# Optimization experiments

Hardware: AMD Instinct MI355X
Metric: run time of the kernel (lower is better)

The kernel has to match this reference:

```python
import jax, jax.numpy as jnp
import numpy as np

N, E, H, C = 50000, 800000, 4, 32   # nodes, edges, heads, per-head channels
HID, LAT, G = H * C, 32, 128        # hidden, latent, num graphs
IN_DIM = 64
NEG_SLOPE = 0.2
BN_EPS = 1e-5


def setup_inputs() -> dict:
    key = jax.random.key(0)
    ks = jax.random.split(key, 20)
    inp = {
        "x": jax.random.normal(ks[0], (N, IN_DIM), jnp.float32),
        "edge_index": jax.random.randint(ks[1], (2, E), 0, N, jnp.int32),
        "batch": jnp.sort(jax.random.randint(ks[2], (N,), 0, G, jnp.int32)),
        # layer 0
        "W0": jax.random.normal(ks[3], (IN_DIM, HID), jnp.float32) * (1.0 / np.sqrt(IN_DIM)),
        "a_src0": jax.random.normal(ks[4], (H, C), jnp.float32) * 0.1,
        "a_dst0": jax.random.normal(ks[5], (H, C), jnp.float32) * 0.1,
        "b0": jnp.zeros((HID,), jnp.float32),
        # layer 1
        "W1": jax.random.normal(ks[6], (HID, HID), jnp.float32) * (1.0 / np.sqrt(HID)),
        "a_src1": jax.random.normal(ks[7], (H, C), jnp.float32) * 0.1,
        "a_dst1": jax.random.normal(ks[8], (H, C), jnp.float32) * 0.1,
        "b1": jnp.zeros((HID,), jnp.float32),
        # layer 2
        "W2": jax.random.normal(ks[9], (HID, HID), jnp.float32) * (1.0 / np.sqrt(HID)),
        "a_src2": jax.random.normal(ks[10], (H, C), jnp.float32) * 0.1,
        "a_dst2": jax.random.normal(ks[11], (H, C), jnp.float32) * 0.1,
        "b2": jnp.zeros((HID,), jnp.float32),
        # head
        "fc_w": jax.random.normal(ks[12], (HID, LAT), jnp.float32) * (1.0 / np.sqrt(HID)),
        "fc_b": jnp.zeros((LAT,), jnp.float32),
        "bn_g": jnp.ones((LAT,), jnp.float32),
        "bn_b": jnp.zeros((LAT,), jnp.float32),
    }
    return inp


def _gat_conv(x, src, dst, W, a_src, a_dst, b):
    n = x.shape[0]
    h = (x @ W).reshape(n, H, C)                      # [N,H,C]
    alpha_s = jnp.einsum("nhc,hc->nh", h, a_src)       # [N,H]
    alpha_d = jnp.einsum("nhc,hc->nh", h, a_dst)
    e = jax.nn.leaky_relu(alpha_s[src] + alpha_d[dst], NEG_SLOPE)  # [E',H]
    # scatter-softmax over incoming edges of each dst node
    m = jax.ops.segment_max(e, dst, num_segments=n)
    m = jnp.where(jnp.isfinite(m), m, 0.0)
    ex = jnp.exp(e - m[dst])
    denom = jax.ops.segment_sum(ex, dst, num_segments=n)
    alpha = ex / (denom[dst] + 1e-16)                  # [E',H]
    out = jax.ops.segment_sum(alpha[:, :, None] * h[src], dst, num_segments=n)
    return out.reshape(n, H * C) + b


def reference(x, edge_index, batch, W0, a_src0, a_dst0, b0, W1, a_src1, a_dst1, b1,
              W2, a_src2, a_dst2, b2, fc_w, fc_b, bn_g, bn_b):
    # PyG GATConv default add_self_loops=True
    loop = jnp.arange(N, dtype=edge_index.dtype)
    src = jnp.concatenate([edge_index[0], loop])
    dst = jnp.concatenate([edge_index[1], loop])

    h = x
    for (W, a_s, a_d, b) in ((W0, a_src0, a_dst0, b0),
                             (W1, a_src1, a_dst1, b1),
                             (W2, a_src2, a_dst2, b2)):
        h = _gat_conv(h, src, dst, W, a_s, a_d, b)
        h = jax.nn.leaky_relu(h, NEG_SLOPE)  # dropout is identity in eval

    pooled = jax.ops.segment_sum(h, batch, num_segments=G)  # global_add_pool -> [G,HID]
    out = pooled @ fc_w + fc_b
    # BatchNorm1d in eval mode with running_mean=0, running_var=1
    out = bn_g * out * (1.0 / np.sqrt(1.0 + BN_EPS)) + bn_b
    return out
```

## Files before the change

kernel.cpp:

```cpp
#include <hip/hip_runtime.h>
#include <hip/hip_bf16.h>
#include <float.h>

#define NEG 0.2f

__device__ __forceinline__ float leaky(float x) { return x > 0.0f ? x : NEG * x; }

__device__ __forceinline__ unsigned short f2bf(float f) {
  unsigned x = __float_as_uint(f);
  unsigned r = (x + 0x7fffu + ((x >> 16) & 1u)) >> 16;
  return (unsigned short)r;
}

__device__ __forceinline__ float2 bf2f2(unsigned u) {
  float2 r;
  r.x = __uint_as_float(u << 16);
  r.y = __uint_as_float(u & 0xffff0000u);
  return r;
}

__global__ void zero_kernel(int* __restrict__ p, int n) {
  int i = blockIdx.x * blockDim.x + threadIdx.x;
  int stride = gridDim.x * blockDim.x;
  for (; i < n; i += stride) p[i] = 0;
}

__global__ void count_kernel(const int* __restrict__ ei, int* __restrict__ deg, int E, int N) {
  int i = blockIdx.x * blockDim.x + threadIdx.x;
  if (i >= E + N) return;
  int dst = (i < E) ? ei[E + i] : (i - E);
  atomicAdd(&deg[dst], 1);
}

__global__ __launch_bounds__(1024) void scan_block_kernel(const int* __restrict__ deg,
                                                          int* __restrict__ row_start,
                                                          int* __restrict__ sums, int n) {
  __shared__ int buf[1024];
  int t = threadIdx.x;
  int idx = blockIdx.x * 1024 + t;
  int x = (idx < n) ? deg[idx] : 0;
  int v = x;
  buf[t] = v;
  __syncthreads();
  for (int off = 1; off < 1024; off <<= 1) {
    int a = (t >= off) ? buf[t - off] : 0;
    __syncthreads();
    v += a;
    buf[t] = v;
    __syncthreads();
  }
  if (idx < n) row_start[idx] = v - x;
  if (t == 1023) sums[blockIdx.x] = v;
}

__global__ __launch_bounds__(1024) void scan_sums_kernel(int* __restrict__ sums,
                                                         int* __restrict__ row_start,
                                                         int nch, int n) {
  __shared__ int buf[1024];
  int t = threadIdx.x;
  int x = (t < nch) ? sums[t] : 0;
  int v = x;
  buf[t] = v;
  __syncthreads();
  for (int off = 1; off < 1024; off <<= 1) {
    int a = (t >= off) ? buf[t - off] : 0;
    __syncthreads();
    v += a;
    buf[t] = v;
    __syncthreads();
  }
  if (t < nch) sums[t] = v - x;
  if (t == 1023) row_start[n] = v;
}

__global__ __launch_bounds__(1024) void scan_add_kernel(int* __restrict__ row_start,
                                                        const int* __restrict__ sums, int n) {
  int idx = blockIdx.x * 1024 + threadIdx.x;
  if (idx < n) row_start[idx] += sums[blockIdx.x];
}

__global__ void fill_kernel(const int* __restrict__ ei, int* __restrict__ cursor,
                            const int* __restrict__ row_start, int* __restrict__ csr_src,
                            int* __restrict__ csr_dst, int E, int N) {
  int i = blockIdx.x * blockDim.x + threadIdx.x;
  if (i >= E + N) return;
  int src, dst;
  if (i < E) { src = ei[i]; dst = ei[E + i]; } else { src = dst = i - E; }
  int pos = atomicAdd(&cursor[dst], 1);
  int slot = row_start[dst] + pos;
  csr_src[slot] = src;
  csr_dst[slot] = dst;
}

__global__ __launch_bounds__(256) void gemm_kernel(const float* __restrict__ X,
                                                   const float* __restrict__ W,
                                                   unsigned short* __restrict__ Hb,
                                                   const float* __restrict__ a_src,
                                                   const float* __restrict__ a_dst,
                                                   float* __restrict__ as_arr,
                                                   float* __restrict__ ad_arr,
                                                   int nrows, int K) {
  __shared__ float Xs[64][36];
  __shared__ float Ws[32][132];
  int t = threadIdx.x;
  int row0 = blockIdx.x * 64;
  int tcol = t & 31;
  int trow = t >> 5;
  float acc[8][4];
#pragma unroll
  for (int i = 0; i < 8; ++i)
#pragma unroll
    for (int j = 0; j < 4; ++j) acc[i][j] = 0.0f;

  for (int kb = 0; kb < K; kb += 32) {
#pragma unroll
    for (int p = 0; p < 2; ++p) {
      int flat = t + p * 256;
      int r = flat >> 3;
      int kq = (flat & 7) * 4;
      float4 v = make_float4(0.f, 0.f, 0.f, 0.f);
      int gr = row0 + r;
      if (gr < nrows) v = *(const float4*)(X + (size_t)gr * K + kb + kq);
      *(float4*)(&Xs[r][kq]) = v;
    }
#pragma unroll
    for (int p = 0; p < 4; ++p) {
      int flat = t + p * 256;
      int r = flat >> 5;
      int cq = (flat & 31) * 4;
      float4 v = *(const float4*)(W + (size_t)(kb + r) * 128 + cq);
      *(float4*)(&Ws[r][cq]) = v;
    }
    __syncthreads();
#pragma unroll
    for (int kk = 0; kk < 32; kk += 4) {
      float4 xv[8];
#pragma unroll
      for (int i = 0; i < 8; ++i) xv[i] = *(const float4*)(&Xs[trow + 8 * i][kk]);
#pragma unroll
      for (int q = 0; q < 4; ++q) {
        float4 wv = *(const float4*)(&Ws[kk + q][tcol * 4]);
#pragma unroll
        for (int i = 0; i < 8; ++i) {
          float xq = (q == 0) ? xv[i].x : (q == 1) ? xv[i].y : (q == 2) ? xv[i].z : xv[i].w;
          acc[i][0] += xq * wv.x;
          acc[i][1] += xq * wv.y;
          acc[i][2] += xq * wv.z;
          acc[i][3] += xq * wv.w;
        }
      }
    }
    __syncthreads();
  }

  float4 as4 = *(const float4*)(a_src + tcol * 4);
  float4 ad4 = *(const float4*)(a_dst + tcol * 4);
  float ps[8], pd[8];
#pragma unroll
  for (int i = 0; i < 8; ++i) {
    int r = row0 + trow + 8 * i;
    if (r < nrows) {
      union { unsigned short u[4]; uint2 v; } pk;
      pk.u[0] = f2bf(acc[i][0]);
      pk.u[1] = f2bf(acc[i][1]);
      pk.u[2] = f2bf(acc[i][2]);
      pk.u[3] = f2bf(acc[i][3]);
      *(uint2*)(Hb + (size_t)r * 128 + tcol * 4) = pk.v;
    }
    ps[i] = acc[i][0] * as4.x + acc[i][1] * as4.y + acc[i][2] * as4.z + acc[i][3] * as4.w;
    pd[i] = acc[i][0] * ad4.x + acc[i][1] * ad4.y + acc[i][2] * ad4.z + acc[i][3] * ad4.w;
  }
#pragma unroll
  for (int off = 1; off < 8; off <<= 1) {
#pragma unroll
    for (int i = 0; i < 8; ++i) {
      ps[i] += __shfl_xor(ps[i], off);
      pd[i] += __shfl_xor(pd[i], off);
    }
  }
  if ((tcol & 7) == 0) {
    int head = tcol >> 3;
#pragma unroll
    for (int i = 0; i < 8; ++i) {
      int r = row0 + trow + 8 * i;
      if (r < nrows) {
        as_arr[(size_t)r * 4 + head] = ps[i];
        ad_arr[(size_t)r * 4 + head] = pd[i];
      }
    }
  }
}

__global__ __launch_bounds__(256) void ecomp_kernel(const int* __restrict__ csr_src,
                                                    const int* __restrict__ csr_dst,
                                                    const float* __restrict__ as_arr,
                                                    const float* __restrict__ ad_arr,
                                                    float* __restrict__ earr, int Etot) {
  int i = blockIdx.x * 256 + threadIdx.x;
  if (i >= Etot) return;
  int s = csr_src[i];
  int d = csr_dst[i];
  float4 a = *(const float4*)(as_arr + (size_t)s * 4);
  float4 b = *(const float4*)(ad_arr + (size_t)d * 4);
  float4 e;
  e.x = __expf(fminf(leaky(a.x + b.x), 80.f));
  e.y = __expf(fminf(leaky(a.y + b.y), 80.f));
  e.z = __expf(fminf(leaky(a.z + b.z), 80.f));
  e.w = __expf(fminf(leaky(a.w + b.w), 80.f));
  *(float4*)(earr + (size_t)i * 4) = e;
}

template <int POOL>
__global__ __launch_bounds__(256) void agg_kernel(const unsigned short* __restrict__ Hb,
                                                  const float* __restrict__ earr,
                                                  const int* __restrict__ csr_src,
                                                  const int* __restrict__ row_start,
                                                  const float* __restrict__ bias,
                                                  float* __restrict__ xnext,
                                                  const int* __restrict__ batch,
                                                  float* __restrict__ pooled, int N) {
  int wid = threadIdx.x >> 6;
  int lane = threadIdx.x & 63;
  int n = blockIdx.x * 4 + wid;
  if (n >= N) return;
  int rs = row_start[n], re = row_start[n + 1];
  int head = lane >> 4;

  const unsigned* hp = (const unsigned*)Hb + lane;
  const float* ep = earr + head;
  float denom = 0.f, acc0 = 0.f, acc1 = 0.f;
  int i = rs;
  for (; i + 4 <= re; i += 4) {
    int s0 = csr_src[i], s1 = csr_src[i + 1], s2 = csr_src[i + 2], s3 = csr_src[i + 3];
    float e0 = ep[(size_t)i * 4];
    float e1 = ep[(size_t)(i + 1) * 4];
    float e2 = ep[(size_t)(i + 2) * 4];
    float e3 = ep[(size_t)(i + 3) * 4];
    unsigned u0 = hp[(size_t)s0 * 64];
    unsigned u1 = hp[(size_t)s1 * 64];
    unsigned u2 = hp[(size_t)s2 * 64];
    unsigned u3 = hp[(size_t)s3 * 64];
    denom += (e0 + e1) + (e2 + e3);
    float2 f;
    f = bf2f2(u0); acc0 += e0 * f.x; acc1 += e0 * f.y;
    f = bf2f2(u1); acc0 += e1 * f.x; acc1 += e1 * f.y;
    f = bf2f2(u2); acc0 += e2 * f.x; acc1 += e2 * f.y;
    f = bf2f2(u3); acc0 += e3 * f.x; acc1 += e3 * f.y;
  }
  for (; i < re; ++i) {
    int s0 = csr_src[i];
    float e0 = ep[(size_t)i * 4];
    unsigned u0 = hp[(size_t)s0 * 64];
    float2 f = bf2f2(u0);
    denom += e0;
    acc0 += e0 * f.x;
    acc1 += e0 * f.y;
  }
  float inv = 1.0f / (denom + 1e-16f);
  float2 bv = *(const float2*)(bias + 2 * lane);
  float v0 = leaky(acc0 * inv + bv.x);
  float v1 = leaky(acc1 * inv + bv.y);
  if (POOL) {
    int g = batch[n];
    atomicAdd(&pooled[(size_t)g * 128 + 2 * lane], v0);
    atomicAdd(&pooled[(size_t)g * 128 + 2 * lane + 1], v1);
  } else {
    *(float2*)(xnext + (size_t)n * 128 + 2 * lane) = make_float2(v0, v1);
  }
}

__global__ void head_kernel(const float* __restrict__ pooled, const float* __restrict__ fc_w,
                            const float* __restrict__ fc_b, const float* __restrict__ bn_g,
                            const float* __restrict__ bn_b, float* __restrict__ out, int G) {
  int t = threadIdx.x;
  int g = blockIdx.x * 8 + (t >> 5);
  int j = t & 31;
  if (g >= G) return;
  const float* pr = pooled + (size_t)g * 128;
  float acc = 0.f;
#pragma unroll 8
  for (int k = 0; k < 128; ++k) acc += pr[k] * fc_w[k * 32 + j];
  const float inv = 0.9999950000374997f;
  out[g * 32 + j] = bn_g[j] * (acc + fc_b[j]) * inv + bn_b[j];
}

extern "C" void kernel_launch(void* const* d_in, const int* in_sizes, int n_in,
                              void* d_out, int out_size, void* d_ws, size_t ws_size,
                              hipStream_t stream) {
  const float* x = (const float*)d_in[0];
  const int* ei = (const int*)d_in[1];
  const int* batch = (const int*)d_in[2];
  const float* Wm[3] = {(const float*)d_in[3], (const float*)d_in[7], (const float*)d_in[11]};
  const float* a_s[3] = {(const float*)d_in[4], (const float*)d_in[8], (const float*)d_in[12]};
  const float* a_d[3] = {(const float*)d_in[5], (const float*)d_in[9], (const float*)d_in[13]};
  const float* bb[3] = {(const float*)d_in[6], (const float*)d_in[10], (const float*)d_in[14]};
  const float* fc_w = (const float*)d_in[15];
  const float* fc_b = (const float*)d_in[16];
  const float* bn_g = (const float*)d_in[17];
  const float* bn_b = (const float*)d_in[18];
  float* out = (float*)d_out;

  int N = in_sizes[0] / 64;
  int E = in_sizes[1] / 2;
  int G = out_size / 32;
  int Etot = E + N;

  char* p = (char*)d_ws;
  auto carve = [&](size_t bytes) {
    char* r = p;
    p += (bytes + 255) & ~size_t(255);
    return r;
  };
  int* deg       = (int*)carve((size_t)N * 4);
  int* cursor    = (int*)carve((size_t)N * 4);
  float* pooled  = (float*)carve((size_t)G * 128 * 4);
  int* row_start = (int*)carve((size_t)(N + 1) * 4);
  int* sums      = (int*)carve(4096);
  int* csr_src   = (int*)carve((size_t)Etot * 4);
  int* csr_dst   = (int*)carve((size_t)Etot * 4);
  float* earr    = (float*)carve((size_t)Etot * 4 * 4);
  unsigned short* Hb = (unsigned short*)carve((size_t)N * 128 * 2);
  float* bufX    = (float*)carve((size_t)N * 128 * 4);
  float* as_arr  = (float*)carve((size_t)N * 4 * 4);
  float* ad_arr  = (float*)carve((size_t)N * 4 * 4);

  int nz = (int)(((char*)(pooled + (size_t)G * 128) - (char*)deg) / 4);
  zero_kernel<<<512, 256, 0, stream>>>(deg, nz);

  int egrid = (Etot + 255) / 256;
  count_kernel<<<egrid, 256, 0, stream>>>(ei, deg, E, N);
  int nch = (N + 1023) / 1024;
  scan_block_kernel<<<nch, 1024, 0, stream>>>(deg, row_start, sums, N);
  scan_sums_kernel<<<1, 1024, 0, stream>>>(sums, row_start, nch, N);
  scan_add_kernel<<<nch, 1024, 0, stream>>>(row_start, sums, N);
  fill_kernel<<<egrid, 256, 0, stream>>>(ei, cursor, row_start, csr_src, csr_dst, E, N);

  int ggrid = (N + 63) / 64;
  int ngrid = (N + 3) / 4;

  gemm_kernel<<<ggrid, 256, 0, stream>>>(x, Wm[0], Hb, a_s[0], a_d[0], as_arr, ad_arr, N, 64);
  ecomp_kernel<<<egrid, 256, 0, stream>>>(csr_src, csr_dst, as_arr, ad_arr, earr, Etot);
  agg_kernel<0><<<ngrid, 256, 0, stream>>>(Hb, earr, csr_src, row_start, bb[0],
                                           bufX, nullptr, nullptr, N);
  gemm_kernel<<<ggrid, 256, 0, stream>>>(bufX, Wm[1], Hb, a_s[1], a_d[1], as_arr, ad_arr, N, 128);
  ecomp_kernel<<<egrid, 256, 0, stream>>>(csr_src, csr_dst, as_arr, ad_arr, earr, Etot);
  agg_kernel<0><<<ngrid, 256, 0, stream>>>(Hb, earr, csr_src, row_start, bb[1],
                                           bufX, nullptr, nullptr, N);
  gemm_kernel<<<ggrid, 256, 0, stream>>>(bufX, Wm[2], Hb, a_s[2], a_d[2], as_arr, ad_arr, N, 128);
  ecomp_kernel<<<egrid, 256, 0, stream>>>(csr_src, csr_dst, as_arr, ad_arr, earr, Etot);
  agg_kernel<1><<<ngrid, 256, 0, stream>>>(Hb, earr, csr_src, row_start, bb[2],
                                           nullptr, batch, pooled, N);

  head_kernel<<<(G + 7) / 8, 256, 0, stream>>>(pooled, fc_w, fc_b, bn_g, bn_b, out, G);
}
```

Baseline: 483.1 us.

## Store features and edge weights head-major; aggregate per head with edge-parallel lanes

```diff
diff --git a/kernel.cpp b/kernel.cpp
--- a/kernel.cpp
+++ b/kernel.cpp
@@ -94,7 +94,7 @@
 
 __global__ __launch_bounds__(256) void gemm_kernel(const float* __restrict__ X,
                                                    const float* __restrict__ W,
-                                                   unsigned short* __restrict__ Hb,
+                                                   unsigned short* __restrict__ Hbh,
                                                    const float* __restrict__ a_src,
                                                    const float* __restrict__ a_dst,
                                                    float* __restrict__ as_arr,
@@ -155,6 +155,7 @@
 
   float4 as4 = *(const float4*)(a_src + tcol * 4);
   float4 ad4 = *(const float4*)(a_dst + tcol * 4);
+  int head = tcol >> 3, sub = tcol & 7;
   float ps[8], pd[8];
 #pragma unroll
   for (int i = 0; i < 8; ++i) {
@@ -165,7 +166,7 @@
       pk.u[1] = f2bf(acc[i][1]);
       pk.u[2] = f2bf(acc[i][2]);
       pk.u[3] = f2bf(acc[i][3]);
-      *(uint2*)(Hb + (size_t)r * 128 + tcol * 4) = pk.v;
+      *(uint2*)(Hbh + ((size_t)head * nrows + r) * 32 + sub * 4) = pk.v;
     }
     ps[i] = acc[i][0] * as4.x + acc[i][1] * as4.y + acc[i][2] * as4.z + acc[i][3] * as4.w;
     pd[i] = acc[i][0] * ad4.x + acc[i][1] * ad4.y + acc[i][2] * ad4.z + acc[i][3] * ad4.w;
@@ -178,8 +179,7 @@
       pd[i] += __shfl_xor(pd[i], off);
     }
   }
-  if ((tcol & 7) == 0) {
-    int head = tcol >> 3;
+  if (sub == 0) {
 #pragma unroll
     for (int i = 0; i < 8; ++i) {
       int r = row0 + trow + 8 * i;
@@ -195,77 +195,72 @@
                                                     const int* __restrict__ csr_dst,
                                                     const float* __restrict__ as_arr,
                                                     const float* __restrict__ ad_arr,
-                                                    float* __restrict__ earr, int Etot) {
+                                                    float* __restrict__ eh, int Etot) {
   int i = blockIdx.x * 256 + threadIdx.x;
   if (i >= Etot) return;
   int s = csr_src[i];
   int d = csr_dst[i];
   float4 a = *(const float4*)(as_arr + (size_t)s * 4);
   float4 b = *(const float4*)(ad_arr + (size_t)d * 4);
-  float4 e;
-  e.x = __expf(fminf(leaky(a.x + b.x), 80.f));
-  e.y = __expf(fminf(leaky(a.y + b.y), 80.f));
-  e.z = __expf(fminf(leaky(a.z + b.z), 80.f));
-  e.w = __expf(fminf(leaky(a.w + b.w), 80.f));
-  *(float4*)(earr + (size_t)i * 4) = e;
+  eh[i]                    = __expf(fminf(leaky(a.x + b.x), 80.f));
+  eh[(size_t)Etot + i]     = __expf(fminf(leaky(a.y + b.y), 80.f));
+  eh[(size_t)2 * Etot + i] = __expf(fminf(leaky(a.z + b.z), 80.f));
+  eh[(size_t)3 * Etot + i] = __expf(fminf(leaky(a.w + b.w), 80.f));
 }
 
 template <int POOL>
-__global__ __launch_bounds__(256) void agg_kernel(const unsigned short* __restrict__ Hb,
-                                                  const float* __restrict__ earr,
+__global__ __launch_bounds__(256) void agg_kernel(const unsigned short* __restrict__ Hbh,
+                                                  const float* __restrict__ eh,
                                                   const int* __restrict__ csr_src,
                                                   const int* __restrict__ row_start,
                                                   const float* __restrict__ bias,
                                                   float* __restrict__ xnext,
                                                   const int* __restrict__ batch,
-                                                  float* __restrict__ pooled, int N) {
+                                                  float* __restrict__ pooled,
+                                                  int N, int Etot) {
   int wid = threadIdx.x >> 6;
   int lane = threadIdx.x & 63;
+  int q = lane >> 4, ql = lane & 15;
   int n = blockIdx.x * 4 + wid;
   if (n >= N) return;
   int rs = row_start[n], re = row_start[n + 1];
-  int head = lane >> 4;
-
-  const unsigned* hp = (const unsigned*)Hb + lane;
-  const float* ep = earr + head;
-  float denom = 0.f, acc0 = 0.f, acc1 = 0.f;
-  int i = rs;
-  for (; i + 4 <= re; i += 4) {
-    int s0 = csr_src[i], s1 = csr_src[i + 1], s2 = csr_src[i + 2], s3 = csr_src[i + 3];
-    float e0 = ep[(size_t)i * 4];
-    float e1 = ep[(size_t)(i + 1) * 4];
-    float e2 = ep[(size_t)(i + 2) * 4];
-    float e3 = ep[(size_t)(i + 3) * 4];
-    unsigned u0 = hp[(size_t)s0 * 64];
-    unsigned u1 = hp[(size_t)s1 * 64];
-    unsigned u2 = hp[(size_t)s2 * 64];
-    unsigned u3 = hp[(size_t)s3 * 64];
-    denom += (e0 + e1) + (e2 + e3);
-    float2 f;
-    f = bf2f2(u0); acc0 += e0 * f.x; acc1 += e0 * f.y;
-    f = bf2f2(u1); acc0 += e1 * f.x; acc1 += e1 * f.y;
-    f = bf2f2(u2); acc0 += e2 * f.x; acc1 += e2 * f.y;
-    f = bf2f2(u3); acc0 += e3 * f.x; acc1 += e3 * f.y;
-  }
-  for (; i < re; ++i) {
-    int s0 = csr_src[i];
-    float e0 = ep[(size_t)i * 4];
-    unsigned u0 = hp[(size_t)s0 * 64];
-    float2 f = bf2f2(u0);
-    denom += e0;
-    acc0 += e0 * f.x;
-    acc1 += e0 * f.y;
-  }
-  float inv = 1.0f / (denom + 1e-16f);
-  float2 bv = *(const float2*)(bias + 2 * lane);
-  float v0 = leaky(acc0 * inv + bv.x);
-  float v1 = leaky(acc1 * inv + bv.y);
-  if (POOL) {
-    int g = batch[n];
-    atomicAdd(&pooled[(size_t)g * 128 + 2 * lane], v0);
-    atomicAdd(&pooled[(size_t)g * 128 + 2 * lane + 1], v1);
-  } else {
-    *(float2*)(xnext + (size_t)n * 128 + 2 * lane) = make_float2(v0, v1);
+  int g = POOL ? batch[n] : 0;
+
+#pragma unroll
+  for (int h = 0; h < 4; ++h) {
+    const unsigned* hb = (const unsigned*)Hbh + (size_t)h * N * 16 + ql;
+    const float* ep = eh + (size_t)h * Etot;
+    float acc0 = 0.f, acc1 = 0.f, den = 0.f;
+    for (int i = rs; i < re; i += 8) {
+      int i0 = i + q, i1 = i + 4 + q;
+      int j0 = i0 < re ? i0 : rs;
+      int j1 = i1 < re ? i1 : rs;
+      int s0 = csr_src[j0], s1 = csr_src[j1];
+      float e0 = i0 < re ? ep[j0] : 0.f;
+      float e1 = i1 < re ? ep[j1] : 0.f;
+      unsigned u0 = hb[(size_t)s0 * 16];
+      unsigned u1 = hb[(size_t)s1 * 16];
+      float2 f0 = bf2f2(u0), f1 = bf2f2(u1);
+      den += e0 + e1;
+      acc0 += e0 * f0.x + e1 * f1.x;
+      acc1 += e0 * f0.y + e1 * f1.y;
+    }
+    acc0 += __shfl_xor(acc0, 16); acc0 += __shfl_xor(acc0, 32);
+    acc1 += __shfl_xor(acc1, 16); acc1 += __shfl_xor(acc1, 32);
+    den  += __shfl_xor(den, 16);  den  += __shfl_xor(den, 32);
+    if (q == 0) {
+      float inv = 1.0f / (den + 1e-16f);
+      int ch = h * 32 + 2 * ql;
+      float2 bv = *(const float2*)(bias + ch);
+      float v0 = leaky(acc0 * inv + bv.x);
+      float v1 = leaky(acc1 * inv + bv.y);
+      if (POOL) {
+        atomicAdd(&pooled[(size_t)g * 128 + ch], v0);
+        atomicAdd(&pooled[(size_t)g * 128 + ch + 1], v1);
+      } else {
+        *(float2*)(xnext + (size_t)n * 128 + ch) = make_float2(v0, v1);
+      }
+    }
   }
 }
 
@@ -318,8 +313,8 @@
   int* sums      = (int*)carve(4096);
   int* csr_src   = (int*)carve((size_t)Etot * 4);
   int* csr_dst   = (int*)carve((size_t)Etot * 4);
-  float* earr    = (float*)carve((size_t)Etot * 4 * 4);
-  unsigned short* Hb = (unsigned short*)carve((size_t)N * 128 * 2);
+  float* eh      = (float*)carve((size_t)Etot * 4 * 4);
+  unsigned short* Hbh = (unsigned short*)carve((size_t)N * 128 * 2);
   float* bufX    = (float*)carve((size_t)N * 128 * 4);
   float* as_arr  = (float*)carve((size_t)N * 4 * 4);
   float* ad_arr  = (float*)carve((size_t)N * 4 * 4);
@@ -338,18 +333,18 @@
   int ggrid = (N + 63) / 64;
   int ngrid = (N + 3) / 4;
 
-  gemm_kernel<<<ggrid, 256, 0, stream>>>(x, Wm[0], Hb, a_s[0], a_d[0], as_arr, ad_arr, N, 64);
-  ecomp_kernel<<<egrid, 256, 0, stream>>>(csr_src, csr_dst, as_arr, ad_arr, earr, Etot);
-  agg_kernel<0><<<ngrid, 256, 0, stream>>>(Hb, earr, csr_src, row_start, bb[0],
-                                           bufX, nullptr, nullptr, N);
-  gemm_kernel<<<ggrid, 256, 0, stream>>>(bufX, Wm[1], Hb, a_s[1], a_d[1], as_arr, ad_arr, N, 128);
-  ecomp_kernel<<<egrid, 256, 0, stream>>>(csr_src, csr_dst, as_arr, ad_arr, earr, Etot);
-  agg_kernel<0><<<ngrid, 256, 0, stream>>>(Hb, earr, csr_src, row_start, bb[1],
-                                           bufX, nullptr, nullptr, N);
-  gemm_kernel<<<ggrid, 256, 0, stream>>>(bufX, Wm[2], Hb, a_s[2], a_d[2], as_arr, ad_arr, N, 128);
-  ecomp_kernel<<<egrid, 256, 0, stream>>>(csr_src, csr_dst, as_arr, ad_arr, earr, Etot);
-  agg_kernel<1><<<ngrid, 256, 0, stream>>>(Hb, earr, csr_src, row_start, bb[2],
-                                           nullptr, batch, pooled, N);
+  gemm_kernel<<<ggrid, 256, 0, stream>>>(x, Wm[0], Hbh, a_s[0], a_d[0], as_arr, ad_arr, N, 64);
+  ecomp_kernel<<<egrid, 256, 0, stream>>>(csr_src, csr_dst, as_arr, ad_arr, eh, Etot);
+  agg_kernel<0><<<ngrid, 256, 0, stream>>>(Hbh, eh, csr_src, row_start, bb[0],
+                                           bufX, nullptr, nullptr, N, Etot);
+  gemm_kernel<<<ggrid, 256, 0, stream>>>(bufX, Wm[1], Hbh, a_s[1], a_d[1], as_arr, ad_arr, N, 128);
+  ecomp_kernel<<<egrid, 256, 0, stream>>>(csr_src, csr_dst, as_arr, ad_arr, eh, Etot);
+  agg_kernel<0><<<ngrid, 256, 0, stream>>>(Hbh, eh, csr_src, row_start, bb[1],
+                                           bufX, nullptr, nullptr, N, Etot);
+  gemm_kernel<<<ggrid, 256, 0, stream>>>(bufX, Wm[2], Hbh, a_s[2], a_d[2], as_arr, ad_arr, N, 128);
+  ecomp_kernel<<<egrid, 256, 0, stream>>>(csr_src, csr_dst, as_arr, ad_arr, eh, Etot);
+  agg_kernel<1><<<ngrid, 256, 0, stream>>>(Hbh, eh, csr_src, row_start, bb[2],
+                                           nullptr, batch, pooled, N, Etot);
 
   head_kernel<<<(G + 7) / 8, 256, 0, stream>>>(pooled, fc_w, fc_b, bn_g, bn_b, out, G);
 }
```

New measurement: 594.2 us. 23.0% more time.
